# Kernel optimization log

Hardware: AMD Instinct MI355X
Metric: run time of the kernel (lower is better)

Reference implementation:

```python
import jax, jax.numpy as jnp
import numpy as np


def setup_inputs() -> dict:
    key = jax.random.key(0)
    ks = jax.random.split(key, 12)
    B, N, M, C = 2, 20000, 4096, 6
    S, K, J = 2, 25, 64          # scales, grid cells (2*2+1)^2, neighbors per cell
    Cin = C + 2                   # xy coords concatenated to features
    Cout = 64
    xyz = jax.random.normal(ks[0], (B, N, 3), dtype=jnp.float32)
    feature = jax.random.normal(ks[1], (B, N, C), dtype=jnp.float32)
    new_xyz = jax.random.normal(ks[2], (B, M, 3), dtype=jnp.float32)
    idx = jax.random.randint(ks[3], (S, B, M, K, J), 0, N, dtype=jnp.int32)
    weight = jax.random.uniform(ks[4], (S, B, M, K, J), dtype=jnp.float32)
    conv_w = jax.random.normal(ks[5], (Cout, Cin, K), dtype=jnp.float32) * 0.05
    conv_b = jnp.zeros((Cout,), dtype=jnp.float32)
    mlp_w0 = jax.random.normal(ks[6], (128, S * Cout), dtype=jnp.float32) * 0.05
    mlp_b0 = jnp.zeros((128,), dtype=jnp.float32)
    mlp_w1 = jax.random.normal(ks[7], (256, 128), dtype=jnp.float32) * 0.05
    mlp_b1 = jnp.zeros((256,), dtype=jnp.float32)
    return {"xyz": xyz, "feature": feature, "new_xyz": new_xyz, "idx": idx,
            "weight": weight, "conv_w": conv_w, "conv_b": conv_b,
            "mlp_w0": mlp_w0, "mlp_b0": mlp_b0, "mlp_w1": mlp_w1, "mlp_b1": mlp_b1}


def reference(xyz, feature, new_xyz, idx, weight, conv_w, conv_b,
              mlp_w0, mlp_b0, mlp_w1, mlp_b1):
    # xyz_feature = cat(xy, feature): (B, N, Cin)
    xf = jnp.concatenate([xyz[:, :, :2], feature], axis=-1)
    center2 = new_xyz[:, :, :2]  # (B, M, 2); remaining channels of center are zero

    def per_scale(idx_s, w_s):
        # idx_s, w_s: (B, M, K, J). Gather neighbor features then bilinear-weight.
        gathered = jax.vmap(lambda f, i: f[i])(xf, idx_s)     # (B, M, K, J, Cin)
        nf = jnp.einsum('bmkj,bmkjc->bmkc', w_s, gathered)    # (B, M, K, Cin)
        nf = nf.at[..., :2].add(-center2[:, :, None, :])      # subtract center (xy only)
        # conv2d with kernel (1, K) over the neighbor axis + ReLU
        out = jnp.einsum('bmkc,ock->bom', nf, conv_w) + conv_b[None, :, None]
        return jax.nn.relu(out)                                # (B, Cout, M)

    outs = [per_scale(idx[s], weight[s]) for s in range(idx.shape[0])]
    x = jnp.concatenate(outs, axis=1)                          # (B, S*Cout, M)
    # SharedMLP: 1x1 convs with ReLU (bn=False)
    x = jax.nn.relu(jnp.einsum('bcm,oc->bom', x, mlp_w0) + mlp_b0[None, :, None])
    x = jax.nn.relu(jnp.einsum('bcm,oc->bom', x, mlp_w1) + mlp_b1[None, :, None])
    result_feature = jnp.transpose(x, (0, 2, 1))               # (B, M, 256)
    return new_xyz, result_feature
```

## Files before the change

### kernel.cpp

```cpp
#include <hip/hip_runtime.h>
#include <hip/hip_bf16.h>

#define B 2
#define N 20000
#define M 4096
#define S 2
#define K 25
#define J 64
#define KJ (K*J)
#define TC 32

#define GPB   128
#define NTH   1024

typedef int   iv4 __attribute__((ext_vector_type(4)));
typedef float fv4 __attribute__((ext_vector_type(4)));

template<int CTRL>
__device__ __forceinline__ float dppadd(float x) {
    return x + __int_as_float(
        __builtin_amdgcn_update_dpp(0, __float_as_int(x), CTRL, 0xF, 0xF, true));
}
__device__ __forceinline__ float red8(float x) {
    x = dppadd<0xB1>(x);
    x = dppadd<0x4E>(x);
    x = dppadd<0x141>(x);
    return x;
}

__global__ __launch_bounds__(256) void prep_kernel(
    const float* __restrict__ xyz, const float* __restrict__ feature,
    const float* __restrict__ new_xyz, const float* __restrict__ conv_w,
    const float* __restrict__ w0, const float* __restrict__ w1,
    __hip_bfloat16* __restrict__ xfh, float* __restrict__ conv_wT,
    float* __restrict__ w0T, float* __restrict__ w1T,
    float* __restrict__ wsum, float* __restrict__ out_newxyz) {
    const int T1 = B * N * 8;
    const int T2 = 208 * 64;
    const int T3 = B * M * 3;
    const int T4 = 128 * 128;
    const int T5 = 128 * 256;
    const int T6 = 128;
    int e = blockIdx.x * blockDim.x + threadIdx.x;
    if (e < T1) {
        int r = e >> 3, t = e & 7;
        int b = r / N, rr = r - b * N;
        int plane = t >> 2, tt = t & 3;
        float v = (t < 2) ? xyz[r * 3 + t] : feature[r * 6 + (t - 2)];
        xfh[((size_t)(b * 2 + plane) * N + rr) * 4 + tt] = __float2bfloat16(v);
    } else if (e < T1 + T2) {
        int e2 = e - T1;
        int i4 = e2 >> 8;
        int rem = e2 & 255;
        int o = rem >> 2, t = rem & 3;
        int i = i4 * 4 + t;
        conv_wT[e2] = (i < 200) ? conv_w[o * 200 + (i & 7) * 25 + (i >> 3)] : 0.f;
    } else if (e < T1 + T2 + T3) {
        int e3 = e - T1 - T2;
        out_newxyz[e3] = new_xyz[e3];
    } else if (e < T1 + T2 + T3 + T4) {
        int e4 = e - T1 - T2 - T3;
        int c = e4 >> 7, o = e4 & 127;
        w0T[e4] = w0[o * 128 + c];
    } else if (e < T1 + T2 + T3 + T4 + T5) {
        int e5 = e - T1 - T2 - T3 - T4;
        int c = e5 >> 8, o = e5 & 255;
        w1T[e5] = w1[o * 128 + c];
    } else if (e < T1 + T2 + T3 + T4 + T5 + T6) {
        int e6 = e - T1 - T2 - T3 - T4 - T5;
        int o = e6 & 63, sel = e6 >> 6;
        float s = 0.f;
        for (int k = 0; k < 25; ++k) s += conv_w[o * 200 + sel * 25 + k];
        wsum[e6] = s;
    }
}

struct UD { iv4 ia, ib; fv4 wa, wb; };

__device__ __forceinline__ UD loadu(const int* __restrict__ idx,
                                    const float* __restrict__ weight,
                                    size_t base) {
    UD d;
    d.ia = __builtin_nontemporal_load((const iv4*)(idx + base));
    d.ib = __builtin_nontemporal_load((const iv4*)(idx + base) + 1);
    d.wa = __builtin_nontemporal_load((const fv4*)(weight + base));
    d.wb = __builtin_nontemporal_load((const fv4*)(weight + base) + 1);
    return d;
}

__device__ __forceinline__ void procu(const UD& d, const uint2* chunk, float* ar) {
    const int   ids[8] = {d.ia.x, d.ia.y, d.ia.z, d.ia.w, d.ib.x, d.ib.y, d.ib.z, d.ib.w};
    const float wsv[8] = {d.wa.x, d.wa.y, d.wa.z, d.wa.w, d.wb.x, d.wb.y, d.wb.z, d.wb.w};
    float a0 = 0.f, a1 = 0.f, a2 = 0.f, a3 = 0.f;
    #pragma unroll
    for (int j = 0; j < 8; ++j) {
        const uint2 v = chunk[ids[j]];
        const float w = wsv[j];
        a0 = fmaf(w, __uint_as_float(v.x << 16),         a0);
        a1 = fmaf(w, __uint_as_float(v.x & 0xffff0000u), a1);
        a2 = fmaf(w, __uint_as_float(v.y << 16),         a2);
        a3 = fmaf(w, __uint_as_float(v.y & 0xffff0000u), a3);
    }
    ar[0] = red8(a0); ar[1] = red8(a1); ar[2] = red8(a2); ar[3] = red8(a3);
}

template<int NK>
__device__ __forceinline__ void convp(const float4* __restrict__ wp,
                                      const float (*ar)[4], float* acc2) {
    #pragma unroll
    for (int kk = 0; kk < NK; ++kk) {
        const float4 w4 = wp[(size_t)kk * 128];
        #pragma unroll
        for (int u = 0; u < 4; ++u) {
            acc2[u] = fmaf(w4.x, __shfl(ar[u][0], kk * 8, 64), acc2[u]);
            acc2[u] = fmaf(w4.y, __shfl(ar[u][1], kk * 8, 64), acc2[u]);
            acc2[u] = fmaf(w4.z, __shfl(ar[u][2], kk * 8, 64), acc2[u]);
            acc2[u] = fmaf(w4.w, __shfl(ar[u][3], kk * 8, 64), acc2[u]);
        }
    }
}

__global__ __launch_bounds__(NTH, 4) void gather_conv_kernel(
    const int* __restrict__ idx, const float* __restrict__ weight,
    const float* __restrict__ new_xyz, const uint2* __restrict__ xfp,
    const float* __restrict__ conv_wT, const float* __restrict__ conv_b,
    const float* __restrict__ wsum,
    float* __restrict__ xmidA, float* __restrict__ xmidB) {
    __shared__ uint2 chunk[N];

    const int bid   = blockIdx.x;
    const int plane = bid & 1;
    const int g0    = (bid >> 1) * GPB;
    const int b     = (g0 >> 12) & (B - 1);
    const uint2* src = xfp + (size_t)(b * 2 + plane) * N;

    const int tid = threadIdx.x;
    for (int r = tid; r < N; r += NTH) chunk[r] = src[r];
    __syncthreads();

    const int team = tid >> 6;
    const int lane = tid & 63;
    const float4* cw4 = (const float4*)conv_wT;
    const int cwo = plane * 64 + lane;
    const int lg  = lane >> 3;
    const size_t joff = (size_t)((lane & 7) * 8);

    const float bo  = conv_b[lane];
    const float wsx = wsum[lane];
    const float wsy = wsum[64 + lane];

    const size_t mkJ0 = (size_t)(lg) * J;
    const size_t mkJ1 = (size_t)(8 + lg) * J;
    const size_t mkJ2 = (size_t)(16 + lg) * J;
    const size_t mkJ3 = (size_t)24 * J;

    #pragma unroll 1
    for (int set = 0; set < 2; ++set) {
        const int gbase = g0 + team * 8 + set * 4;
        const size_t gb = (size_t)gbase * KJ + joff;
        float acc2[4] = {0.f, 0.f, 0.f, 0.f};
        float ar[4][4];

        UD d0  = loadu(idx, weight, gb + 0 * KJ + mkJ0);
        UD d1  = loadu(idx, weight, gb + 1 * KJ + mkJ0);
        UD d2  = loadu(idx, weight, gb + 2 * KJ + mkJ0);  procu(d0,  chunk, ar[0]);
        UD d3  = loadu(idx, weight, gb + 3 * KJ + mkJ0);  procu(d1,  chunk, ar[1]);
        UD d4  = loadu(idx, weight, gb + 0 * KJ + mkJ1);  procu(d2,  chunk, ar[2]);
        UD d5  = loadu(idx, weight, gb + 1 * KJ + mkJ1);  procu(d3,  chunk, ar[3]);
        convp<8>(cw4 + (size_t)0 * 1024 + cwo, ar, acc2);
        UD d6  = loadu(idx, weight, gb + 2 * KJ + mkJ1);  procu(d4,  chunk, ar[0]);
        UD d7  = loadu(idx, weight, gb + 3 * KJ + mkJ1);  procu(d5,  chunk, ar[1]);
        UD d8  = loadu(idx, weight, gb + 0 * KJ + mkJ2);  procu(d6,  chunk, ar[2]);
        UD d9  = loadu(idx, weight, gb + 1 * KJ + mkJ2);  procu(d7,  chunk, ar[3]);
        convp<8>(cw4 + (size_t)1 * 1024 + cwo, ar, acc2);
        UD d10 = loadu(idx, weight, gb + 2 * KJ + mkJ2);  procu(d8,  chunk, ar[0]);
        UD d11 = loadu(idx, weight, gb + 3 * KJ + mkJ2);  procu(d9,  chunk, ar[1]);
        UD d12 = loadu(idx, weight, gb + 0 * KJ + mkJ3);  procu(d10, chunk, ar[2]);
        UD d13 = loadu(idx, weight, gb + 1 * KJ + mkJ3);  procu(d11, chunk, ar[3]);
        convp<8>(cw4 + (size_t)2 * 1024 + cwo, ar, acc2);
        UD d14 = loadu(idx, weight, gb + 2 * KJ + mkJ3);  procu(d12, chunk, ar[0]);
        UD d15 = loadu(idx, weight, gb + 3 * KJ + mkJ3);  procu(d13, chunk, ar[1]);
        procu(d14, chunk, ar[2]);
        procu(d15, chunk, ar[3]);
        convp<1>(cw4 + (size_t)3 * 1024 + cwo, ar, acc2);

        if (plane == 0) {
            #pragma unroll
            for (int u = 0; u < 4; ++u) {
                const int g = gbase + u;
                const int m = g & (M - 1);
                const int s = g >> 13;
                const float cx = new_xyz[(b * M + m) * 3 + 0];
                const float cy = new_xyz[(b * M + m) * 3 + 1];
                xmidA[((size_t)(b * M + m)) * 128 + s * 64 + lane]
                    = acc2[u] + bo - cx * wsx - cy * wsy;
            }
        } else {
            #pragma unroll
            for (int u = 0; u < 4; ++u) {
                const int g = gbase + u;
                const int m = g & (M - 1);
                const int s = g >> 13;
                xmidB[((size_t)(b * M + m)) * 128 + s * 64 + lane] = acc2[u];
            }
        }
    }
}

__device__ __forceinline__ void gemm_tile(const float* xs, const float* ws,
                                          int o0, int lc0, float acc[4][4]) {
    for (int c = 0; c < 128; ++c) {
        float4 xv = *(const float4*)&xs[c * 32 + lc0];
        float4 wv = *(const float4*)&ws[c * 128 + o0];
        acc[0][0] = fmaf(wv.x, xv.x, acc[0][0]);
        acc[0][1] = fmaf(wv.x, xv.y, acc[0][1]);
        acc[0][2] = fmaf(wv.x, xv.z, acc[0][2]);
        acc[0][3] = fmaf(wv.x, xv.w, acc[0][3]);
        acc[1][0] = fmaf(wv.y, xv.x, acc[1][0]);
        acc[1][1] = fmaf(wv.y, xv.y, acc[1][1]);
        acc[1][2] = fmaf(wv.y, xv.z, acc[1][2]);
        acc[1][3] = fmaf(wv.y, xv.w, acc[1][3]);
        acc[2][0] = fmaf(wv.z, xv.x, acc[2][0]);
        acc[2][1] = fmaf(wv.z, xv.y, acc[2][1]);
        acc[2][2] = fmaf(wv.z, xv.z, acc[2][2]);
        acc[2][3] = fmaf(wv.z, xv.w, acc[2][3]);
        acc[3][0] = fmaf(wv.w, xv.x, acc[3][0]);
        acc[3][1] = fmaf(wv.w, xv.y, acc[3][1]);
        acc[3][2] = fmaf(wv.w, xv.z, acc[3][2]);
        acc[3][3] = fmaf(wv.w, xv.w, acc[3][3]);
    }
}

__global__ __launch_bounds__(256) void mlp01_kernel(
    const float* __restrict__ xmidA, const float* __restrict__ xmidB,
    const float* __restrict__ w0T, const float* __restrict__ b0,
    const float* __restrict__ w1T, const float* __restrict__ b1,
    float* __restrict__ out_rf) {
    __shared__ float ws[128 * 128];
    __shared__ float xs[128 * 32];

    int tid = threadIdx.x;
    int col0 = blockIdx.x * TC;
    int og = tid >> 3, cg = tid & 7;
    int o0 = og * 4, lc0 = cg * 4;

    {
        const float4* w4 = (const float4*)w0T;
        float4* ws4 = (float4*)ws;
        #pragma unroll
        for (int i = 0; i < 16; ++i) ws4[tid + 256 * i] = w4[tid + 256 * i];
    }
    {
        const float4* xa4 = (const float4*)(xmidA + (size_t)col0 * 128);
        const float4* xb4 = (const float4*)(xmidB + (size_t)col0 * 128);
        #pragma unroll
        for (int r = tid; r < 1024; r += 256) {
            int lc = r >> 5, c4 = r & 31;
            float4 va = xa4[lc * 32 + c4];
            float4 vb = xb4[lc * 32 + c4];
            int c = c4 * 4;
            xs[(c + 0) * 32 + lc] = fmaxf(va.x + vb.x, 0.f);
            xs[(c + 1) * 32 + lc] = fmaxf(va.y + vb.y, 0.f);
            xs[(c + 2) * 32 + lc] = fmaxf(va.z + vb.z, 0.f);
            xs[(c + 3) * 32 + lc] = fmaxf(va.w + vb.w, 0.f);
        }
    }
    __syncthreads();

    float acc[4][4];
    #pragma unroll
    for (int i = 0; i < 4; ++i) {
        float bv = b0[o0 + i];
        #pragma unroll
        for (int u = 0; u < 4; ++u) acc[i][u] = bv;
    }
    gemm_tile(xs, ws, o0, lc0, acc);
    __syncthreads();

    #pragma unroll
    for (int i = 0; i < 4; ++i)
        #pragma unroll
        for (int u = 0; u < 4; ++u)
            xs[(o0 + i) * 32 + lc0 + u] = fmaxf(acc[i][u], 0.f);
    for (int i = tid; i < 4096; i += 256) {
        int c = i >> 5, q = i & 31;
        *(float4*)&ws[c * 128 + q * 4] = *(const float4*)&w1T[c * 256 + q * 4];
    }
    __syncthreads();

    #pragma unroll
    for (int i = 0; i < 4; ++i) {
        float bv = b1[o0 + i];
        #pragma unroll
        for (int u = 0; u < 4; ++u) acc[i][u] = bv;
    }
    gemm_tile(xs, ws, o0, lc0, acc);
    #pragma unroll
    for (int u = 0; u < 4; ++u) {
        float4 v = make_float4(fmaxf(acc[0][u], 0.f), fmaxf(acc[1][u], 0.f),
                               fmaxf(acc[2][u], 0.f), fmaxf(acc[3][u], 0.f));
        *(float4*)&out_rf[(size_t)(col0 + lc0 + u) * 256 + o0] = v;
    }
    __syncthreads();

    for (int i = tid; i < 4096; i += 256) {
        int c = i >> 5, q = i & 31;
        *(float4*)&ws[c * 128 + q * 4] = *(const float4*)&w1T[c * 256 + 128 + q * 4];
    }
    __syncthreads();

    #pragma unroll
    for (int i = 0; i < 4; ++i) {
        float bv = b1[128 + o0 + i];
        #pragma unroll
        for (int u = 0; u < 4; ++u) acc[i][u] = bv;
    }
    gemm_tile(xs, ws, o0, lc0, acc);
    #pragma unroll
    for (int u = 0; u < 4; ++u) {
        float4 v = make_float4(fmaxf(acc[0][u], 0.f), fmaxf(acc[1][u], 0.f),
                               fmaxf(acc[2][u], 0.f), fmaxf(acc[3][u], 0.f));
        *(float4*)&out_rf[(size_t)(col0 + lc0 + u) * 256 + 128 + o0] = v;
    }
}

extern "C" void kernel_launch(void* const* d_in, const int* in_sizes, int n_in,
                              void* d_out, int out_size, void* d_ws, size_t ws_size,
                              hipStream_t stream) {
    const float* xyz     = (const float*)d_in[0];
    const float* feature = (const float*)d_in[1];
    const float* new_xyz = (const float*)d_in[2];
    const int*   idx     = (const int*)  d_in[3];
    const float* weight  = (const float*)d_in[4];
    const float* conv_w  = (const float*)d_in[5];
    const float* conv_b  = (const float*)d_in[6];
    const float* mlp_w0  = (const float*)d_in[7];
    const float* mlp_b0  = (const float*)d_in[8];
    const float* mlp_w1  = (const float*)d_in[9];
    const float* mlp_b1  = (const float*)d_in[10];

    float* out    = (float*)d_out;
    float* out_rf = out + (size_t)B * M * 3;

    float* wsf = (float*)d_ws;
    __hip_bfloat16* xfh = (__hip_bfloat16*)wsf;
    float* conv_wT = wsf + 160000;
    float* xmidA   = conv_wT + 13312;
    float* w0T     = xmidA + 1048576;
    float* w1T     = w0T + 16384;
    float* wsum    = w1T + 32768;
    float* xmidB   = wsum + 128;

    {
        int total = 320000 + 13312 + 24576 + 16384 + 32768 + 128;
        int blocks = (total + 255) / 256;
        prep_kernel<<<blocks, 256, 0, stream>>>(xyz, feature, new_xyz, conv_w,
                                                mlp_w0, mlp_w1,
                                                xfh, conv_wT, w0T, w1T, wsum, out);
    }
    {
        int blocks = 2 * (S * B * M) / GPB;
        gather_conv_kernel<<<blocks, NTH, 0, stream>>>(idx, weight, new_xyz,
                                                       (const uint2*)xfh,
                                                       conv_wT, conv_b, wsum,
                                                       xmidA, xmidB);
    }
    {
        mlp01_kernel<<<(B * M) / TC, 256, 0, stream>>>(xmidA, xmidB,
                                                       w0T, mlp_b0,
                                                       w1T, mlp_b1, out_rf);
    }
}
```

Baseline: 363.4 us.

## Use readlane broadcasts, loop over k-groups, and repartition tail k across lanes

Replaces the __shfl broadcasts in the conv accumulation with scalar readlane, since the source lane index is uniform across the wave. The hand-pipelined 16-load sequence becomes a loop over three k-groups that does not unroll, which removes the explicit software prefetching. The last k (index 24), previously handled with 7/8 of lanes idle, is now split so 16 lanes per group cover 4 groups at once, using a 16-wide DPP reduction. This cuts idle lanes and shuffle cost, but it may lose the load/compute overlap the manual pipelining provided.

```diff
diff --git a/kernel.cpp b/kernel.cpp
--- a/kernel.cpp
+++ b/kernel.cpp
@@ -26,6 +26,16 @@
     x = dppadd<0x4E>(x);
     x = dppadd<0x141>(x);
     return x;
+}
+__device__ __forceinline__ float red16(float x) {
+    x = dppadd<0xB1>(x);
+    x = dppadd<0x4E>(x);
+    x = dppadd<0x141>(x);
+    x = dppadd<0x140>(x);
+    return x;
+}
+__device__ __forceinline__ float brd(float x, int l) {
+    return __int_as_float(__builtin_amdgcn_readlane(__float_as_int(x), l));
 }
 
 __global__ __launch_bounds__(256) void prep_kernel(
@@ -104,18 +114,17 @@
     ar[0] = red8(a0); ar[1] = red8(a1); ar[2] = red8(a2); ar[3] = red8(a3);
 }
 
-template<int NK>
-__device__ __forceinline__ void convp(const float4* __restrict__ wp,
-                                      const float (*ar)[4], float* acc2) {
-    #pragma unroll
-    for (int kk = 0; kk < NK; ++kk) {
+__device__ __forceinline__ void convp8(const float4* __restrict__ wp,
+                                       const float (*ar)[4], float* acc2) {
+    #pragma unroll
+    for (int kk = 0; kk < 8; ++kk) {
         const float4 w4 = wp[(size_t)kk * 128];
         #pragma unroll
         for (int u = 0; u < 4; ++u) {
-            acc2[u] = fmaf(w4.x, __shfl(ar[u][0], kk * 8, 64), acc2[u]);
-            acc2[u] = fmaf(w4.y, __shfl(ar[u][1], kk * 8, 64), acc2[u]);
-            acc2[u] = fmaf(w4.z, __shfl(ar[u][2], kk * 8, 64), acc2[u]);
-            acc2[u] = fmaf(w4.w, __shfl(ar[u][3], kk * 8, 64), acc2[u]);
+            acc2[u] = fmaf(w4.x, brd(ar[u][0], kk * 8), acc2[u]);
+            acc2[u] = fmaf(w4.y, brd(ar[u][1], kk * 8), acc2[u]);
+            acc2[u] = fmaf(w4.z, brd(ar[u][2], kk * 8), acc2[u]);
+            acc2[u] = fmaf(w4.w, brd(ar[u][3], kk * 8), acc2[u]);
         }
     }
 }
@@ -149,40 +158,51 @@
     const float wsx = wsum[lane];
     const float wsy = wsum[64 + lane];
 
-    const size_t mkJ0 = (size_t)(lg) * J;
-    const size_t mkJ1 = (size_t)(8 + lg) * J;
-    const size_t mkJ2 = (size_t)(16 + lg) * J;
-    const size_t mkJ3 = (size_t)24 * J;
-
     #pragma unroll 1
     for (int set = 0; set < 2; ++set) {
         const int gbase = g0 + team * 8 + set * 4;
-        const size_t gb = (size_t)gbase * KJ + joff;
         float acc2[4] = {0.f, 0.f, 0.f, 0.f};
         float ar[4][4];
 
-        UD d0  = loadu(idx, weight, gb + 0 * KJ + mkJ0);
-        UD d1  = loadu(idx, weight, gb + 1 * KJ + mkJ0);
-        UD d2  = loadu(idx, weight, gb + 2 * KJ + mkJ0);  procu(d0,  chunk, ar[0]);
-        UD d3  = loadu(idx, weight, gb + 3 * KJ + mkJ0);  procu(d1,  chunk, ar[1]);
-        UD d4  = loadu(idx, weight, gb + 0 * KJ + mkJ1);  procu(d2,  chunk, ar[2]);
-        UD d5  = loadu(idx, weight, gb + 1 * KJ + mkJ1);  procu(d3,  chunk, ar[3]);
-        convp<8>(cw4 + (size_t)0 * 1024 + cwo, ar, acc2);
-        UD d6  = loadu(idx, weight, gb + 2 * KJ + mkJ1);  procu(d4,  chunk, ar[0]);
-        UD d7  = loadu(idx, weight, gb + 3 * KJ + mkJ1);  procu(d5,  chunk, ar[1]);
-        UD d8  = loadu(idx, weight, gb + 0 * KJ + mkJ2);  procu(d6,  chunk, ar[2]);
-        UD d9  = loadu(idx, weight, gb + 1 * KJ + mkJ2);  procu(d7,  chunk, ar[3]);
-        convp<8>(cw4 + (size_t)1 * 1024 + cwo, ar, acc2);
-        UD d10 = loadu(idx, weight, gb + 2 * KJ + mkJ2);  procu(d8,  chunk, ar[0]);
-        UD d11 = loadu(idx, weight, gb + 3 * KJ + mkJ2);  procu(d9,  chunk, ar[1]);
-        UD d12 = loadu(idx, weight, gb + 0 * KJ + mkJ3);  procu(d10, chunk, ar[2]);
-        UD d13 = loadu(idx, weight, gb + 1 * KJ + mkJ3);  procu(d11, chunk, ar[3]);
-        convp<8>(cw4 + (size_t)2 * 1024 + cwo, ar, acc2);
-        UD d14 = loadu(idx, weight, gb + 2 * KJ + mkJ3);  procu(d12, chunk, ar[0]);
-        UD d15 = loadu(idx, weight, gb + 3 * KJ + mkJ3);  procu(d13, chunk, ar[1]);
-        procu(d14, chunk, ar[2]);
-        procu(d15, chunk, ar[3]);
-        convp<1>(cw4 + (size_t)3 * 1024 + cwo, ar, acc2);
+        #pragma unroll 1
+        for (int p = 0; p < 3; ++p) {
+            const size_t mkJ = (size_t)(p * 8 + lg) * J;
+            #pragma unroll
+            for (int u = 0; u < 4; ++u) {
+                const size_t base = (size_t)(gbase + u) * KJ + mkJ + joff;
+                UD d = loadu(idx, weight, base);
+                procu(d, chunk, ar[u]);
+            }
+            convp8(cw4 + (size_t)(p * 8) * 128 + cwo, ar, acc2);
+        }
+
+        {
+            const int u16 = lane >> 4, sub = lane & 15;
+            const size_t base3 = (size_t)(gbase + u16) * KJ + (size_t)24 * J + sub * 4;
+            const iv4 i4v = __builtin_nontemporal_load((const iv4*)(idx + base3));
+            const fv4 w4v = __builtin_nontemporal_load((const fv4*)(weight + base3));
+            const int   ids3[4] = {i4v.x, i4v.y, i4v.z, i4v.w};
+            const float ws3[4]  = {w4v.x, w4v.y, w4v.z, w4v.w};
+            float a0 = 0.f, a1 = 0.f, a2 = 0.f, a3 = 0.f;
+            #pragma unroll
+            for (int j = 0; j < 4; ++j) {
+                const uint2 v = chunk[ids3[j]];
+                const float w = ws3[j];
+                a0 = fmaf(w, __uint_as_float(v.x << 16),         a0);
+                a1 = fmaf(w, __uint_as_float(v.x & 0xffff0000u), a1);
+                a2 = fmaf(w, __uint_as_float(v.y << 16),         a2);
+                a3 = fmaf(w, __uint_as_float(v.y & 0xffff0000u), a3);
+            }
+            a0 = red16(a0); a1 = red16(a1); a2 = red16(a2); a3 = red16(a3);
+            const float4 wk = cw4[(size_t)24 * 128 + cwo];
+            #pragma unroll
+            for (int u = 0; u < 4; ++u) {
+                acc2[u] = fmaf(wk.x, brd(a0, u * 16), acc2[u]);
+                acc2[u] = fmaf(wk.y, brd(a1, u * 16), acc2[u]);
+                acc2[u] = fmaf(wk.z, brd(a2, u * 16), acc2[u]);
+                acc2[u] = fmaf(wk.w, brd(a3, u * 16), acc2[u]);
+            }
+        }
 
         if (plane == 0) {
             #pragma unroll
```

New measurement: 313.2 us. 13.8% less time.
